# Performance work log

Measured on AMD Instinct MI355X. Metric: run time of the kernel, lower is better.

Reference implementation:

```python
import jax, jax.numpy as jnp
import numpy as np

HEADS = 16
EMB_DIM = 1024
MODEL_DIM = 1024
HEAD_DIM = EMB_DIM // HEADS
N, SEQ = 4, 1024


def setup_inputs() -> dict:
    key = jax.random.key(0)
    ks = jax.random.split(key, 9)
    s = 1.0 / np.sqrt(EMB_DIM)
    return {
        "query_inputs": jax.random.normal(ks[0], (N, SEQ, EMB_DIM), jnp.float32),
        "key_inputs": jax.random.normal(ks[1], (N, SEQ, EMB_DIM), jnp.float32),
        "value_inputs": jax.random.normal(ks[2], (N, SEQ, EMB_DIM), jnp.float32),
        "Wq": jax.random.normal(ks[3], (MODEL_DIM, EMB_DIM), jnp.float32) * s,
        "bq": jax.random.normal(ks[4], (MODEL_DIM,), jnp.float32) * s,
        "Wk": jax.random.normal(ks[5], (MODEL_DIM, EMB_DIM), jnp.float32) * s,
        "bk": jax.random.normal(ks[6], (MODEL_DIM,), jnp.float32) * s,
        "Wv": jax.random.normal(ks[7], (MODEL_DIM, EMB_DIM), jnp.float32) * s,
        "bv": jax.random.normal(ks[8], (MODEL_DIM,), jnp.float32) * s,
    }


def reference(query_inputs, key_inputs, value_inputs, Wq, bq, Wk, bk, Wv, bv):
    n = query_inputs.shape[0]
    qi = query_inputs.reshape(n, -1, query_inputs.shape[-1])
    ki = key_inputs.reshape(n, -1, key_inputs.shape[-1])
    vi = value_inputs.reshape(n, -1, value_inputs.shape[-1])
    q = qi @ Wq.T + bq  # (n, L, model_dim)
    k = ki @ Wk.T + bk
    v = vi @ Wv.T + bv
    L = q.shape[1]
    # Faithful to original (q/v swapped role): 'values'<-q, 'queries'<-v
    values = q.reshape(n, L, HEADS, HEAD_DIM)
    keys = k.reshape(n, L, HEADS, HEAD_DIM)
    queries = v.reshape(n, L, HEADS, HEAD_DIM)
    energy = jnp.einsum('nqhd,nkhd->nhqk', queries, keys)
    attention = jax.nn.softmax(energy / jnp.sqrt(jnp.float32(EMB_DIM)), axis=3)
    out = jnp.einsum('nhql,nlhd->nqhd', attention, values).reshape(n, L, HEADS * HEAD_DIM)
    return out
```

## Files before the change

kernel.cpp:

```cpp
#include <hip/hip_runtime.h>


typedef unsigned short u16;
typedef __attribute__((ext_vector_type(8))) short bf16x8;
typedef __attribute__((ext_vector_type(4))) float f32x4;

#define S_LEN 1024
#define EMB 1024
#define HEADS 16
#define HD 64

__device__ __forceinline__ u16 f2bf(float f) {
    unsigned int u = __float_as_uint(f);
    u = (u + 0x7fffu + ((u >> 16) & 1u)) >> 16;
    return (u16)u;
}

typedef const __attribute__((address_space(1))) unsigned glob_u32;
typedef __attribute__((address_space(3))) unsigned lds_u32;
__device__ __forceinline__ void gld16(const u16* g, u16* l) {
    __builtin_amdgcn_global_load_lds((glob_u32*)g, (lds_u32*)l, 16, 0, 0);
}

struct CvtArgs {
    const float* src[6];
    u16* dst[6];
};

__global__ __launch_bounds__(256) void cvt_f32_bf16(CvtArgs a)
{
    const long total = (3L << 20) + (3L << 18);
    for (long i = (long)blockIdx.x * 256 + threadIdx.x; i < total;
         i += (long)gridDim.x * 256) {
        int arr, off;
        if (i < (3L << 20)) { arr = (int)(i >> 20); off = (int)(i & ((1 << 20) - 1)); }
        else { long j = i - (3L << 20); arr = 3 + (int)(j >> 18); off = (int)(j & ((1 << 18) - 1)); }
        float4 v = reinterpret_cast<const float4*>(a.src[arr])[off];
        ushort4 o; o.x = f2bf(v.x); o.y = f2bf(v.y); o.z = f2bf(v.z); o.w = f2bf(v.w);
        reinterpret_cast<ushort4*>(a.dst[arr])[off] = o;
    }
}

__global__ __launch_bounds__(256) void qkv_gemm_bf16(
    const u16* __restrict__ Xq, const u16* __restrict__ Xk, const u16* __restrict__ Xv,
    const u16* __restrict__ Wq, const u16* __restrict__ Wk, const u16* __restrict__ Wv,
    const float* __restrict__ Bq, const float* __restrict__ Bk, const float* __restrict__ Bv,
    u16* __restrict__ vt, u16* __restrict__ katt, u16* __restrict__ qatt)
{
    const int proj = blockIdx.z;
    const u16* X  = (proj == 0) ? Xq : (proj == 1) ? Xk : Xv;
    const u16* W  = (proj == 0) ? Wq : (proj == 1) ? Wk : Wv;
    const float* Bp = (proj == 0) ? Bq : (proj == 1) ? Bk : Bv;

    const int gm0 = blockIdx.x * 128;
    const int gn0 = blockIdx.y * 128;
    const int tid  = threadIdx.x;
    const int lane = tid & 63;
    const int wave = tid >> 6;
    const int wm = wave >> 1, wn = wave & 1;
    const int l15 = lane & 15, l4 = lane >> 4;

    __shared__ u16 As[4][128 * 32];
    __shared__ u16 Bs[4][128 * 32];

    f32x4 acc[4][4];
    #pragma unroll
    for (int i = 0; i < 4; ++i)
        #pragma unroll
        for (int j = 0; j < 4; ++j) { f32x4 z = {0.f,0.f,0.f,0.f}; acc[i][j] = z; }

    const int r0 = tid >> 2,         cc0 = tid & 3;
    const int r1 = (tid + 256) >> 2, cc1 = (tid + 256) & 3;
    const u16* gA0 = X + (size_t)(gm0 + r0) * EMB + cc0 * 8;
    const u16* gA1 = X + (size_t)(gm0 + r1) * EMB + cc1 * 8;
    const u16* gB0 = W + (size_t)(gn0 + r0) * EMB + cc0 * 8;
    const u16* gB1 = W + (size_t)(gn0 + r1) * EMB + cc1 * 8;

    auto stage = [&](int buf, int ktile) {
        const int k0 = ktile * 32;
        u16* a = &As[buf][0] + wave * 512;
        u16* b = &Bs[buf][0] + wave * 512;
        gld16(gA0 + k0, a);
        gld16(gA1 + k0, a + 2048);
        gld16(gB0 + k0, b);
        gld16(gB1 + k0, b + 2048);
    };

    auto compute = [&](int kt) {
        const u16* A = &As[kt & 3][0];
        const u16* B = &Bs[kt & 3][0];
        bf16x8 af[4], bfr[4];
        #pragma unroll
        for (int m = 0; m < 4; ++m)
            af[m] = *reinterpret_cast<const bf16x8*>(&A[(wm * 64 + m * 16 + l15) * 32 + l4 * 8]);
        #pragma unroll
        for (int n = 0; n < 4; ++n)
            bfr[n] = *reinterpret_cast<const bf16x8*>(&B[(wn * 64 + n * 16 + l15) * 32 + l4 * 8]);
        #pragma unroll
        for (int m = 0; m < 4; ++m)
            #pragma unroll
            for (int n = 0; n < 4; ++n)
                acc[m][n] = __builtin_amdgcn_mfma_f32_16x16x32_bf16(af[m], bfr[n], acc[m][n], 0, 0, 0);
    };

    stage(0, 0);
    stage(1, 1);
    stage(2, 2);

    for (int kt = 0; kt < 30; ++kt) {
        asm volatile("s_waitcnt vmcnt(8)" ::: "memory");
        __builtin_amdgcn_s_barrier();
        if (kt <= 28) stage((kt + 3) & 3, kt + 3);
        compute(kt);
    }
    asm volatile("s_waitcnt vmcnt(4)" ::: "memory");
    __builtin_amdgcn_s_barrier();
    compute(30);
    asm volatile("s_waitcnt vmcnt(0)" ::: "memory");
    __builtin_amdgcn_s_barrier();
    compute(31);

    #pragma unroll
    for (int n = 0; n < 4; ++n) {
        const int col = gn0 + wn * 64 + n * 16 + l15;
        const float bias = Bp[col];
        const int h = col >> 6, d = col & 63;
        #pragma unroll
        for (int m = 0; m < 4; ++m) {
            #pragma unroll
            for (int r = 0; r < 4; ++r) {
                const int rowg = gm0 + wm * 64 + m * 16 + l4 * 4 + r;
                const int nb = rowg >> 10, s = rowg & 1023;
                const u16 val = f2bf(acc[m][n][r] + bias);
                const int nh = nb * HEADS + h;
                if (proj == 0)       vt  [((size_t)nh * HD + d) * S_LEN + s] = val;
                else if (proj == 1)  katt[((size_t)nh * S_LEN + s) * HD + d] = val;
                else                 qatt[((size_t)nh * S_LEN + s) * HD + d] = val;
            }
        }
    }
}

__global__ __launch_bounds__(256) void qkv_gemm_f32(
    const float* __restrict__ Xq, const float* __restrict__ Xk, const float* __restrict__ Xv,
    const float* __restrict__ Wq, const float* __restrict__ Wk, const float* __restrict__ Wv,
    const float* __restrict__ Bq, const float* __restrict__ Bk, const float* __restrict__ Bv,
    u16* __restrict__ vt, u16* __restrict__ katt, u16* __restrict__ qatt)
{
    const int proj = blockIdx.z;
    const float* X = (proj == 0) ? Xq : (proj == 1) ? Xk : Xv;
    const float* W = (proj == 0) ? Wq : (proj == 1) ? Wk : Wv;
    const float* Bp = (proj == 0) ? Bq : (proj == 1) ? Bk : Bv;

    const int gm0 = blockIdx.x * 128;
    const int gn0 = blockIdx.y * 128;
    const int tid  = threadIdx.x;
    const int lane = tid & 63;
    const int wave = tid >> 6;
    const int wm = wave >> 1, wn = wave & 1;
    const int l15 = lane & 15, l4 = lane >> 4;

    __shared__ u16 As[128 * 40];
    __shared__ u16 Bs[128 * 40];

    f32x4 acc[4][4];
    #pragma unroll
    for (int i = 0; i < 4; ++i)
        #pragma unroll
        for (int j = 0; j < 4; ++j) { f32x4 z = {0.f,0.f,0.f,0.f}; acc[i][j] = z; }

    const int srow = tid >> 3;
    const int skc  = (tid & 7) * 4;

    for (int kt = 0; kt < 32; ++kt) {
        const int k0 = kt * 32;
        #pragma unroll
        for (int p = 0; p < 4; ++p) {
            const int row = p * 32 + srow;
            float4 a = *reinterpret_cast<const float4*>(&X[(size_t)(gm0 + row) * EMB + k0 + skc]);
            float4 b = *reinterpret_cast<const float4*>(&W[(size_t)(gn0 + row) * EMB + k0 + skc]);
            ushort4 ua; ua.x = f2bf(a.x); ua.y = f2bf(a.y); ua.z = f2bf(a.z); ua.w = f2bf(a.w);
            ushort4 ub; ub.x = f2bf(b.x); ub.y = f2bf(b.y); ub.z = f2bf(b.z); ub.w = f2bf(b.w);
            *reinterpret_cast<ushort4*>(&As[row * 40 + skc]) = ua;
            *reinterpret_cast<ushort4*>(&Bs[row * 40 + skc]) = ub;
        }
        __syncthreads();

        bf16x8 af[4], bfr[4];
        #pragma unroll
        for (int m = 0; m < 4; ++m)
            af[m] = *reinterpret_cast<const bf16x8*>(&As[(wm * 64 + m * 16 + l15) * 40 + l4 * 8]);
        #pragma unroll
        for (int n = 0; n < 4; ++n)
            bfr[n] = *reinterpret_cast<const bf16x8*>(&Bs[(wn * 64 + n * 16 + l15) * 40 + l4 * 8]);

        #pragma unroll
        for (int m = 0; m < 4; ++m)
            #pragma unroll
            for (int n = 0; n < 4; ++n)
                acc[m][n] = __builtin_amdgcn_mfma_f32_16x16x32_bf16(af[m], bfr[n], acc[m][n], 0, 0, 0);
        __syncthreads();
    }

    #pragma unroll
    for (int n = 0; n < 4; ++n) {
        const int col = gn0 + wn * 64 + n * 16 + l15;
        const float bias = Bp[col];
        const int h = col >> 6, d = col & 63;
        #pragma unroll
        for (int m = 0; m < 4; ++m) {
            #pragma unroll
            for (int r = 0; r < 4; ++r) {
                const int rowg = gm0 + wm * 64 + m * 16 + l4 * 4 + r;
                const int nb = rowg >> 10, s = rowg & 1023;
                const u16 val = f2bf(acc[m][n][r] + bias);
                const int nh = nb * HEADS + h;
                if (proj == 0)       vt  [((size_t)nh * HD + d) * S_LEN + s] = val;
                else if (proj == 1)  katt[((size_t)nh * S_LEN + s) * HD + d] = val;
                else                 qatt[((size_t)nh * S_LEN + s) * HD + d] = val;
            }
        }
    }
}

__global__ __launch_bounds__(256) void attn_kernel(
    const u16* __restrict__ qatt, const u16* __restrict__ katt,
    const u16* __restrict__ vt, float* __restrict__ out)
{
    const int qb = blockIdx.x;
    const int nh = blockIdx.y;
    const int tid  = threadIdx.x;
    const int lane = tid & 63;
    const int wave = tid >> 6;
    const int l15 = lane & 15, l4 = lane >> 4;
    const int q0 = qb * 64;
    const int waveQ = wave * 16;

    __shared__ u16 Ks[2][64 * 64];
    __shared__ u16 Vs[2][64 * 64];
    __shared__ u16 Ps[4 * 16 * 72];

    const size_t qbase = (size_t)nh * S_LEN * HD + (size_t)(q0 + waveQ + l15) * HD;
    const bf16x8 qf0 = *reinterpret_cast<const bf16x8*>(&qatt[qbase + l4 * 8]);
    const bf16x8 qf1 = *reinterpret_cast<const bf16x8*>(&qatt[qbase + 32 + l4 * 8]);

    const int r8  = lane >> 3;
    const int ccg = (lane & 7) ^ r8;
    const int row0 = wave * 8 + r8;
    const int row1 = 32 + row0;
    const u16* gK = katt + (size_t)nh * S_LEN * HD;
    const u16* gV = vt   + (size_t)nh * HD * S_LEN;
    const u16* gK0 = gK + (size_t)row0 * HD + ccg * 8;
    const u16* gK1 = gK + (size_t)row1 * HD + ccg * 8;
    const u16* gV0 = gV + (size_t)row0 * S_LEN + ccg * 8;
    const u16* gV1 = gV + (size_t)row1 * S_LEN + ccg * 8;

    f32x4 accO[4];
    #pragma unroll
    for (int i = 0; i < 4; ++i) { f32x4 z = {0.f,0.f,0.f,0.f}; accO[i] = z; }
    float lsum[4] = {0.f, 0.f, 0.f, 0.f};
    const float scale = 0.03125f;

    {
        u16* kb = &Ks[0][0] + wave * 512;
        u16* vb = &Vs[0][0] + wave * 512;
        gld16(gK0, kb);          gld16(gK1, kb + 2048);
        gld16(gV0, vb);          gld16(gV1, vb + 2048);
    }
    __syncthreads();

    for (int kt = 0; kt < 16; ++kt) {
        const int cur = kt & 1;
        if (kt < 15) {
            const size_t kOff = (size_t)(kt + 1) * 64 * HD;
            const size_t vOff = (size_t)(kt + 1) * 64;
            u16* kb = &Ks[cur ^ 1][0] + wave * 512;
            u16* vb = &Vs[cur ^ 1][0] + wave * 512;
            gld16(gK0 + kOff, kb);       gld16(gK1 + kOff, kb + 2048);
            gld16(gV0 + vOff, vb);       gld16(gV1 + vOff, vb + 2048);
        }

        char* KsB = reinterpret_cast<char*>(&Ks[cur][0]);
        char* VsB = reinterpret_cast<char*>(&Vs[cur][0]);

        float pvals[4][4];
        #pragma unroll
        for (int kb = 0; kb < 4; ++kb) {
            const int krow = kb * 16 + l15;
            const int sw = krow & 7;
            bf16x8 kf0 = *reinterpret_cast<const bf16x8*>(KsB + krow * 128 + ((l4 ^ sw) << 4));
            bf16x8 kf1 = *reinterpret_cast<const bf16x8*>(KsB + krow * 128 + (((l4 + 4) ^ sw) << 4));
            f32x4 sacc = {0.f, 0.f, 0.f, 0.f};
            sacc = __builtin_amdgcn_mfma_f32_16x16x32_bf16(qf0, kf0, sacc, 0, 0, 0);
            sacc = __builtin_amdgcn_mfma_f32_16x16x32_bf16(qf1, kf1, sacc, 0, 0, 0);
            #pragma unroll
            for (int r = 0; r < 4; ++r) {
                const float pv = __expf(sacc[r] * scale);
                pvals[kb][r] = pv;
                lsum[r] += pv;
            }
        }

        u16* pw = &Ps[wave * 16 * 72];
        #pragma unroll
        for (int r = 0; r < 4; ++r) {
            const int prow = l4 * 4 + r;
            #pragma unroll
            for (int kb = 0; kb < 4; ++kb)
                pw[prow * 72 + kb * 16 + l15] = f2bf(pvals[kb][r]);
        }
        asm volatile("s_waitcnt lgkmcnt(0)" ::: "memory");
        __builtin_amdgcn_sched_barrier(0);

        const u16* pr = &Ps[wave * 16 * 72 + l15 * 72];
        const bf16x8 pf0 = *reinterpret_cast<const bf16x8*>(&pr[l4 * 8]);
        const bf16x8 pf1 = *reinterpret_cast<const bf16x8*>(&pr[32 + l4 * 8]);

        #pragma unroll
        for (int db = 0; db < 4; ++db) {
            const int vrow = db * 16 + l15;
            const int sw = vrow & 7;
            bf16x8 vf0 = *reinterpret_cast<const bf16x8*>(VsB + vrow * 128 + ((l4 ^ sw) << 4));
            bf16x8 vf1 = *reinterpret_cast<const bf16x8*>(VsB + vrow * 128 + (((l4 + 4) ^ sw) << 4));
            accO[db] = __builtin_amdgcn_mfma_f32_16x16x32_bf16(pf0, vf0, accO[db], 0, 0, 0);
            accO[db] = __builtin_amdgcn_mfma_f32_16x16x32_bf16(pf1, vf1, accO[db], 0, 0, 0);
        }
        __syncthreads();
    }

    #pragma unroll
    for (int r = 0; r < 4; ++r) {
        float s = lsum[r];
        #pragma unroll
        for (int msk = 1; msk < 16; msk <<= 1) s += __shfl_xor(s, msk);
        lsum[r] = 1.0f / s;
    }

    const int n = nh >> 4, h = nh & 15;
    #pragma unroll
    for (int db = 0; db < 4; ++db) {
        const int d = h * 64 + db * 16 + l15;
        #pragma unroll
        for (int r = 0; r < 4; ++r) {
            const int s = q0 + waveQ + l4 * 4 + r;
            out[(size_t)n * S_LEN * EMB + (size_t)s * EMB + d] = accO[db][r] * lsum[r];
        }
    }
}

extern "C" void kernel_launch(void* const* d_in, const int* in_sizes, int n_in,
                              void* d_out, int out_size, void* d_ws, size_t ws_size,
                              hipStream_t stream)
{
    const float* Xq = (const float*)d_in[0];
    const float* Xk = (const float*)d_in[1];
    const float* Xv = (const float*)d_in[2];
    const float* Wq = (const float*)d_in[3];
    const float* bq = (const float*)d_in[4];
    const float* Wk = (const float*)d_in[5];
    const float* bk = (const float*)d_in[6];
    const float* Wv = (const float*)d_in[7];
    const float* bv = (const float*)d_in[8];
    float* out = (float*)d_out;

    const size_t M4 = (size_t)4 * 1024 * 1024;
    const size_t M1 = (size_t)1024 * 1024;

    u16* vt   = (u16*)d_ws;
    u16* katt = vt + M4;
    u16* qatt = katt + M4;

    const size_t need = (3 * M4 + 3 * M4 + 3 * M1) * sizeof(u16);

    if (ws_size >= need) {
        u16* Xqb = qatt + M4;
        u16* Xkb = Xqb + M4;
        u16* Xvb = Xkb + M4;
        u16* Wqb = Xvb + M4;
        u16* Wkb = Wqb + M1;
        u16* Wvb = Wkb + M1;

        CvtArgs ca;
        ca.src[0] = Xq; ca.src[1] = Xk; ca.src[2] = Xv;
        ca.src[3] = Wq; ca.src[4] = Wk; ca.src[5] = Wv;
        ca.dst[0] = Xqb; ca.dst[1] = Xkb; ca.dst[2] = Xvb;
        ca.dst[3] = Wqb; ca.dst[4] = Wkb; ca.dst[5] = Wvb;
        cvt_f32_bf16<<<2048, 256, 0, stream>>>(ca);

        qkv_gemm_bf16<<<dim3(32, 8, 3), 256, 0, stream>>>(
            Xqb, Xkb, Xvb, Wqb, Wkb, Wvb, bq, bk, bv, vt, katt, qatt);
    } else {
        qkv_gemm_f32<<<dim3(32, 8, 3), 256, 0, stream>>>(
            Xq, Xk, Xv, Wq, Wk, Wv, bq, bk, bv, vt, katt, qatt);
    }

    attn_kernel<<<dim3(16, 64), 256, 0, stream>>>(qatt, katt, vt, out);
}
```

Baseline: 215.2 us.

## Use triple-buffered swizzled LDS in projection GEMM and raise MFMA priority

The projection GEMM goes from four LDS stages to three. The main loop is manually unrolled by three with fixed buffer indices and waits at vmcnt(4). Global-to-LDS loads now place 16-byte chunks with an XOR swizzle that matches the fragment reads, which is meant to reduce LDS bank conflicts. s_setprio wraps the MFMA blocks in both the GEMM and the attention kernel so waves doing matrix math get issue priority. The shallower prefetch depth may expose more memory latency, but the smaller LDS footprint may allow higher occupancy.

```diff
diff --git a/kernel.cpp b/kernel.cpp
--- a/kernel.cpp
+++ b/kernel.cpp
@@ -60,8 +60,8 @@
     const int wm = wave >> 1, wn = wave & 1;
     const int l15 = lane & 15, l4 = lane >> 4;
 
-    __shared__ u16 As[4][128 * 32];
-    __shared__ u16 Bs[4][128 * 32];
+    __shared__ u16 As[3][128 * 32];
+    __shared__ u16 Bs[3][128 * 32];
 
     f32x4 acc[4][4];
     #pragma unroll
@@ -69,12 +69,12 @@
         #pragma unroll
         for (int j = 0; j < 4; ++j) { f32x4 z = {0.f,0.f,0.f,0.f}; acc[i][j] = z; }
 
-    const int r0 = tid >> 2,         cc0 = tid & 3;
-    const int r1 = (tid + 256) >> 2, cc1 = (tid + 256) & 3;
-    const u16* gA0 = X + (size_t)(gm0 + r0) * EMB + cc0 * 8;
-    const u16* gA1 = X + (size_t)(gm0 + r1) * EMB + cc1 * 8;
-    const u16* gB0 = W + (size_t)(gn0 + r0) * EMB + cc0 * 8;
-    const u16* gB1 = W + (size_t)(gn0 + r1) * EMB + cc1 * 8;
+    const int rr  = tid >> 2;
+    const int ccg = (tid & 3) ^ ((tid >> 3) & 3);
+    const u16* gA0 = X + (size_t)(gm0 + rr) * EMB + ccg * 8;
+    const u16* gA1 = X + (size_t)(gm0 + 64 + rr) * EMB + ccg * 8;
+    const u16* gB0 = W + (size_t)(gn0 + rr) * EMB + ccg * 8;
+    const u16* gB1 = W + (size_t)(gn0 + 64 + rr) * EMB + ccg * 8;
 
     auto stage = [&](int buf, int ktile) {
         const int k0 = ktile * 32;
@@ -86,39 +86,50 @@
         gld16(gB1 + k0, b + 2048);
     };
 
-    auto compute = [&](int kt) {
-        const u16* A = &As[kt & 3][0];
-        const u16* B = &Bs[kt & 3][0];
+    const int swz = (l15 >> 1) & 3;
+    auto compute = [&](int buf) {
+        const u16* A = &As[buf][0];
+        const u16* B = &Bs[buf][0];
         bf16x8 af[4], bfr[4];
         #pragma unroll
         for (int m = 0; m < 4; ++m)
-            af[m] = *reinterpret_cast<const bf16x8*>(&A[(wm * 64 + m * 16 + l15) * 32 + l4 * 8]);
+            af[m] = *reinterpret_cast<const bf16x8*>(&A[(wm * 64 + m * 16 + l15) * 32 + (l4 ^ swz) * 8]);
         #pragma unroll
         for (int n = 0; n < 4; ++n)
-            bfr[n] = *reinterpret_cast<const bf16x8*>(&B[(wn * 64 + n * 16 + l15) * 32 + l4 * 8]);
+            bfr[n] = *reinterpret_cast<const bf16x8*>(&B[(wn * 64 + n * 16 + l15) * 32 + (l4 ^ swz) * 8]);
+        __builtin_amdgcn_s_setprio(1);
         #pragma unroll
         for (int m = 0; m < 4; ++m)
             #pragma unroll
             for (int n = 0; n < 4; ++n)
                 acc[m][n] = __builtin_amdgcn_mfma_f32_16x16x32_bf16(af[m], bfr[n], acc[m][n], 0, 0, 0);
+        __builtin_amdgcn_s_setprio(0);
     };
 
     stage(0, 0);
     stage(1, 1);
-    stage(2, 2);
-
-    for (int kt = 0; kt < 30; ++kt) {
-        asm volatile("s_waitcnt vmcnt(8)" ::: "memory");
+
+    #pragma unroll 1
+    for (int base = 0; base < 30; base += 3) {
+        asm volatile("s_waitcnt vmcnt(4)" ::: "memory");
         __builtin_amdgcn_s_barrier();
-        if (kt <= 28) stage((kt + 3) & 3, kt + 3);
-        compute(kt);
+        stage(2, base + 2);
+        compute(0);
+        asm volatile("s_waitcnt vmcnt(4)" ::: "memory");
+        __builtin_amdgcn_s_barrier();
+        stage(0, base + 3);
+        compute(1);
+        asm volatile("s_waitcnt vmcnt(4)" ::: "memory");
+        __builtin_amdgcn_s_barrier();
+        stage(1, base + 4);
+        compute(2);
     }
     asm volatile("s_waitcnt vmcnt(4)" ::: "memory");
     __builtin_amdgcn_s_barrier();
-    compute(30);
+    compute(0);
     asm volatile("s_waitcnt vmcnt(0)" ::: "memory");
     __builtin_amdgcn_s_barrier();
-    compute(31);
+    compute(1);
 
     #pragma unroll
     for (int n = 0; n < 4; ++n) {
@@ -291,8 +302,10 @@
             bf16x8 kf0 = *reinterpret_cast<const bf16x8*>(KsB + krow * 128 + ((l4 ^ sw) << 4));
             bf16x8 kf1 = *reinterpret_cast<const bf16x8*>(KsB + krow * 128 + (((l4 + 4) ^ sw) << 4));
             f32x4 sacc = {0.f, 0.f, 0.f, 0.f};
+            __builtin_amdgcn_s_setprio(1);
             sacc = __builtin_amdgcn_mfma_f32_16x16x32_bf16(qf0, kf0, sacc, 0, 0, 0);
             sacc = __builtin_amdgcn_mfma_f32_16x16x32_bf16(qf1, kf1, sacc, 0, 0, 0);
+            __builtin_amdgcn_s_setprio(0);
             #pragma unroll
             for (int r = 0; r < 4; ++r) {
                 const float pv = __expf(sacc[r] * scale);
@@ -316,6 +329,7 @@
         const bf16x8 pf0 = *reinterpret_cast<const bf16x8*>(&pr[l4 * 8]);
         const bf16x8 pf1 = *reinterpret_cast<const bf16x8*>(&pr[32 + l4 * 8]);
 
+        __builtin_amdgcn_s_setprio(1);
         #pragma unroll
         for (int db = 0; db < 4; ++db) {
             const int vrow = db * 16 + l15;
@@ -325,6 +339,7 @@
             accO[db] = __builtin_amdgcn_mfma_f32_16x16x32_bf16(pf0, vf0, accO[db], 0, 0, 0);
             accO[db] = __builtin_amdgcn_mfma_f32_16x16x32_bf16(pf1, vf1, accO[db], 0, 0, 0);
         }
+        __builtin_amdgcn_s_setprio(0);
         __syncthreads();
     }
 
```

Result: no change. 211.4 us (-1.8%).
